# Kernel optimization log

Measured on AMD Instinct MI355X. Metric: run time of the kernel, lower is better.

## Reference

```python
import jax, jax.numpy as jnp
import numpy as np

NODES_PER_GRAPH = 1430  # hard-coded stride in the original forward
GENE0 = 1421            # first gene node index per graph
N_HEADS = 9


def gcn_conv(x, W, b, src, dst, n):
    """PyG-style GCNConv: D^-1/2 (A+I) D^-1/2 X W + b (self-loops added)."""
    h = x @ W  # [N, out]
    ones = jnp.ones(src.shape, jnp.float32)
    deg = jax.ops.segment_sum(ones, dst, num_segments=n) + 1.0  # +1 self-loop
    dinv = jax.lax.rsqrt(deg)
    norm = dinv[src] * dinv[dst]  # [E]
    agg = jax.ops.segment_sum(norm[:, None] * h[src], dst, num_segments=n)
    agg = agg + (dinv * dinv)[:, None] * h  # self-loop contribution
    return agg + b


def setup_inputs() -> dict:
    key = jax.random.key(0)
    ks = jax.random.split(key, 8)
    n_graphs = 512
    n = NODES_PER_GRAPH * n_graphs  # 732160 nodes
    e = n * 8                        # avg degree 8
    x = jax.random.normal(ks[0], (n, 1), jnp.float32)
    edge_index = jax.random.randint(ks[1], (2, e), 0, n, jnp.int32)
    y = jnp.zeros((n_graphs * N_HEADS,), jnp.int32)  # only y.size(0) is used
    W1 = jax.random.normal(ks[2], (1, 16), jnp.float32) * 0.5
    b1 = jnp.zeros((16,), jnp.float32)
    W2 = jax.random.normal(ks[3], (16, 16), jnp.float32) * 0.25
    b2 = jnp.zeros((16,), jnp.float32)
    fw1 = jax.random.normal(ks[4], (N_HEADS, 16, 8), jnp.float32) * 0.25
    fb1 = jnp.zeros((N_HEADS, 8), jnp.float32)
    fw2 = jax.random.normal(ks[5], (N_HEADS, 8, 1), jnp.float32) * 0.35
    fb2 = jnp.zeros((N_HEADS, 1), jnp.float32)
    return {"x": x, "edge_index": edge_index, "y": y, "W1": W1, "b1": b1,
            "W2": W2, "b2": b2, "fw1": fw1, "fb1": fb1, "fw2": fw2, "fb2": fb2}


def reference(x, edge_index, y, W1, b1, W2, b2, fw1, fb1, fw2, fb2):
    n = x.shape[0]
    src, dst = edge_index[0], edge_index[1]
    h = jax.nn.relu(gcn_conv(x, W1, b1, src, dst, n))
    # F.dropout(p=0.4) treated as identity (deterministic eval reference)
    h = jax.nn.relu(gcn_conv(h, W2, b2, src, dst, n))
    n_graphs = y.shape[0] // N_HEADS
    # fused version of the per-gene gather loop: idx[g, k] = 1421+g + k*1430
    idx = (GENE0 + jnp.arange(N_HEADS)[:, None]
           + jnp.arange(n_graphs)[None, :] * NODES_PER_GRAPH)  # [9, G]
    g = h[idx]  # [9, G, 16]
    z = jax.nn.relu(jnp.einsum('gnf,gfh->gnh', g, fw1) + fb1[:, None, :])
    pred = jnp.einsum('gnh,gho->gno', z, fw2) + fb2[:, None, :]  # [9, G, 1]
    return tuple(pred[i] for i in range(N_HEADS))
```

## Files before the change

### kernel.cpp

```cpp
#include <hip/hip_runtime.h>

#define NODES 1430
#define GENE0 1421
#define NHEADS 9
#define BHIST 1024
#define GMAX 64

__device__ __forceinline__ float frelu(float v) { return v > 0.f ? v : 0.f; }

__global__ __launch_bounds__(BHIST, 4)
void k_hist(const int* __restrict__ esrc, const int* __restrict__ edst,
            unsigned int* __restrict__ copies,
            int* __restrict__ gene_cnt, int* __restrict__ gene_src,
            unsigned int* __restrict__ flagw,
            int e, int K, int R, int n, int hbins, int hwords) {
    extern __shared__ unsigned int lds[];
    int id = blockIdx.x;
    int k, r;
    if ((K & 7) == 0) {
        int xcd = id & 7;
        int slot = id >> 3;
        int cin = slot / R;
        k = xcd * (K >> 3) + cin;
        r = slot - cin * R;
    } else {
        k = id / R;
        r = id - k * R;
    }
    const int tid = threadIdx.x;
    {
        uint4* l4 = (uint4*)lds;
        const int hw4 = hwords >> 2;
        for (int w = tid; w < hw4; w += BHIST) l4[w] = make_uint4(0, 0, 0, 0);
    }
    __syncthreads();

    const unsigned int lo = (unsigned int)r * (unsigned int)hbins;
    const unsigned int hb = (unsigned int)hbins;
    const int e4 = e >> 2;
    const int Q = (e4 + K - 1) / K;
    const int beg = k * Q;
    const int end = min(beg + Q, e4);
    const int4* ed4 = (const int4*)edst;
    const int len = (end > beg) ? (end - beg) : 0;
    const int eighth = len >> 3;

    auto proc = [&](int4 d4, int j4) {
#pragma unroll
        for (int c = 0; c < 4; c++) {
            unsigned int d = (unsigned int)((&d4.x)[c]);
            unsigned int rel = d - lo;
            if (rel < hb) {
                atomicAdd(&lds[rel >> 3], 1u << ((rel & 7u) * 4u));
                unsigned int graph = d / NODES;
                unsigned int pos = d - graph * NODES;
                if (pos >= GENE0) {
                    int s = esrc[4 * j4 + c];
                    atomicOr(&flagw[(unsigned)s >> 5], 1u << (s & 31));
                    int g = (int)(graph * NHEADS + (pos - GENE0));
                    int p = atomicAdd(gene_cnt + g, 1);
                    if (p < GMAX) gene_src[(g << 6) + p] = s;
                }
            }
        }
    };

    for (int i = tid; i < eighth; i += BHIST) {
        int j0 = beg + i;
        int4 v0 = ed4[j0];
        int4 v1 = ed4[j0 + eighth];
        int4 v2 = ed4[j0 + 2 * eighth];
        int4 v3 = ed4[j0 + 3 * eighth];
        int4 v4 = ed4[j0 + 4 * eighth];
        int4 v5 = ed4[j0 + 5 * eighth];
        int4 v6 = ed4[j0 + 6 * eighth];
        int4 v7 = ed4[j0 + 7 * eighth];
        proc(v0, j0);
        proc(v1, j0 + eighth);
        proc(v2, j0 + 2 * eighth);
        proc(v3, j0 + 3 * eighth);
        proc(v4, j0 + 4 * eighth);
        proc(v5, j0 + 5 * eighth);
        proc(v6, j0 + 6 * eighth);
        proc(v7, j0 + 7 * eighth);
    }
    for (int i = (eighth << 3) + tid; i < len; i += BHIST) {
        proc(ed4[beg + i], beg + i);
    }
    if (k == 0) {
        for (int j = (e4 << 2) + tid; j < e; j += BHIST) {
            unsigned int d = (unsigned int)edst[j];
            unsigned int rel = d - lo;
            if (rel < hb) {
                atomicAdd(&lds[rel >> 3], 1u << ((rel & 7u) * 4u));
                unsigned int graph = d / NODES;
                unsigned int pos = d - graph * NODES;
                if (pos >= GENE0) {
                    int s = esrc[j];
                    atomicOr(&flagw[(unsigned)s >> 5], 1u << (s & 31));
                    int g = (int)(graph * NHEADS + (pos - GENE0));
                    int p = atomicAdd(gene_cnt + g, 1);
                    if (p < GMAX) gene_src[(g << 6) + p] = s;
                }
            }
        }
    }
    __syncthreads();
    int wlimit = (n > (int)lo) ? ((n - (int)lo + 7) >> 3) : 0;
    if (wlimit > hwords) wlimit = hwords;
    int w4 = (wlimit + 3) >> 2;
    uint4* dst4 = (uint4*)(copies + ((size_t)k * R + r) * hwords);
    const uint4* l4 = (const uint4*)lds;
    for (int w = tid; w < w4; w += BHIST) dst4[w] = l4[w];
}

__global__ void k_reduce(const unsigned int* __restrict__ copies,
                         const float* __restrict__ x,
                         float2* __restrict__ dx, float* __restrict__ t,
                         int n, int K, int Wtot) {
    int w = blockIdx.x * blockDim.x + threadIdx.x;
    if (w >= Wtot) return;
    int i0 = w << 3;
    if (i0 >= n) return;
    const unsigned int M = 0x0F0F0F0Fu;
    unsigned int ev[8] = {0, 0, 0, 0, 0, 0, 0, 0};
    unsigned int od[8] = {0, 0, 0, 0, 0, 0, 0, 0};
    int k = 0;
    for (; k + 8 <= K; k += 8) {
#pragma unroll
        for (int s = 0; s < 8; s++) {
            unsigned int u = copies[(size_t)(k + s) * Wtot + w];
            ev[s] += u & M; od[s] += (u >> 4) & M;
        }
    }
    for (; k < K; k++) {
        unsigned int u = copies[(size_t)k * Wtot + w];
        ev[0] += u & M; od[0] += (u >> 4) & M;
    }
    unsigned int evn = ((ev[0] + ev[1]) + (ev[2] + ev[3])) + ((ev[4] + ev[5]) + (ev[6] + ev[7]));
    unsigned int odd = ((od[0] + od[1]) + (od[2] + od[3])) + ((od[4] + od[5]) + (od[6] + od[7]));
    float v[8];
#pragma unroll
    for (int b = 0; b < 4; b++) {
        v[2 * b]     = (float)((evn >> (8 * b)) & 0xFFu);
        v[2 * b + 1] = (float)((odd >> (8 * b)) & 0xFFu);
    }
#pragma unroll
    for (int b = 0; b < 8; b++) v[b] = rsqrtf(v[b] + 1.f);
    float4 z4 = {0.f, 0.f, 0.f, 0.f};
    if (i0 + 7 < n) {
        float4 xa = *(const float4*)(x + i0);
        float4 xb = *(const float4*)(x + i0 + 4);
        float4 p0 = {v[0], v[0] * xa.x, v[1], v[1] * xa.y};
        float4 p1 = {v[2], v[2] * xa.z, v[3], v[3] * xa.w};
        float4 p2 = {v[4], v[4] * xb.x, v[5], v[5] * xb.y};
        float4 p3 = {v[6], v[6] * xb.z, v[7], v[7] * xb.w};
        float4* dst = (float4*)(dx + i0);
        dst[0] = p0; dst[1] = p1; dst[2] = p2; dst[3] = p3;
        *(float4*)(t + i0) = z4;
        *(float4*)(t + i0 + 4) = z4;
    } else {
        for (int b = 0; b < 8; b++)
            if (i0 + b < n) {
                dx[i0 + b] = make_float2(v[b], v[b] * x[i0 + b]);
                t[i0 + b] = 0.f;
            }
    }
}

__global__ __launch_bounds__(256, 8)
void k_l1_scatter(const int* __restrict__ esrc, const int* __restrict__ edst,
                  const float2* __restrict__ dx,
                  const unsigned int* __restrict__ flagw,
                  float* __restrict__ t, int e) {
    const int4* ed4 = (const int4*)edst;
    const int e4 = e >> 2;
    const int tid = threadIdx.x;
    const int base = blockIdx.x * 2048 + tid;

    int4 dv[8];
#pragma unroll
    for (int k = 0; k < 8; k++) {
        int j = base + k * 256;
        dv[k] = (j < e4) ? ed4[j] : make_int4(-1, -1, -1, -1);
    }
    unsigned int hm[8];
#pragma unroll
    for (int k = 0; k < 8; k++) {
        unsigned int m = 0;
#pragma unroll
        for (int c = 0; c < 4; c++) {
            int d = (&dv[k].x)[c];
            unsigned int widx = (d >= 0) ? ((unsigned)d >> 5) : 0u;
            unsigned int fw = flagw[widx];
            if (d >= 0 && ((fw >> (d & 31)) & 1u)) m |= 1u << c;
        }
        hm[k] = m;
    }
#pragma unroll
    for (int k = 0; k < 8; k++) {
        if (hm[k]) {
            int j = base + k * 256;
#pragma unroll
            for (int c = 0; c < 4; c++) {
                if ((hm[k] >> c) & 1u) {
                    int s = esrc[4 * j + c];
                    atomicAdd(t + (&dv[k].x)[c], dx[s].y);
                }
            }
        }
    }
    if (blockIdx.x == 0) {
        for (int j = (e4 << 2) + tid; j < e; j += 256) {
            int d = edst[j];
            if ((flagw[(unsigned)d >> 5] >> (d & 31)) & 1u)
                atomicAdd(t + d, dx[esrc[j]].y);
        }
    }
}

__global__ void k_gene_final(const int* __restrict__ gene_cnt, const int* __restrict__ gene_src,
                             const float* __restrict__ t, const float2* __restrict__ dx,
                             const float* __restrict__ W1, const float* __restrict__ b1,
                             const float* __restrict__ W2, const float* __restrict__ b2,
                             const float* __restrict__ fw1, const float* __restrict__ fb1,
                             const float* __restrict__ fw2, const float* __restrict__ fb2,
                             float* __restrict__ out, int NG, int G) {
    int wid = (blockIdx.x * blockDim.x + threadIdx.x) >> 6;
    int lane = threadIdx.x & 63;
    if (wid >= NG) return;
    int g = wid;
    int graph = g / NHEADS;
    int head = g - graph * NHEADS;
    int node = graph * NODES + GENE0 + head;
    const int c = lane & 15;
    const int slot = lane >> 4;
    int cnt = min(gene_cnt[g], GMAX);

    float w1r[16], b1r[16], w2c[16];
#pragma unroll
    for (int kk = 0; kk < 16; kk++) {
        w1r[kk] = W1[kk];
        b1r[kk] = b1[kk];
        w2c[kk] = W2[kk * 16 + c];
    }
    float2 dn2 = dx[node];

    float acc = 0.f, tsum = 0.f;
    const int base = g << 6;
    for (int i = slot; i < cnt; i += 8) {
        int s0 = gene_src[base + i];
        int i1 = i + 4;
        int s1 = (i1 < cnt) ? gene_src[base + i1] : -1;
        float2 a2 = dx[s0];
        float ta = t[s0];
        float2 b2v = (s1 >= 0) ? dx[s1] : make_float2(0.f, 0.f);
        float tb = (s1 >= 0) ? t[s1] : 0.f;
        tsum += a2.y + b2v.y;
        {
            float us = a2.x * ta + a2.x * a2.y;
            float m = 0.f;
#pragma unroll
            for (int kk = 0; kk < 16; kk++)
                m += frelu(us * w1r[kk] + b1r[kk]) * w2c[kk];
            acc += a2.x * m;
        }
        if (s1 >= 0) {
            float us = b2v.x * tb + b2v.x * b2v.y;
            float m = 0.f;
#pragma unroll
            for (int kk = 0; kk < 16; kk++)
                m += frelu(us * w1r[kk] + b1r[kk]) * w2c[kk];
            acc += b2v.x * m;
        }
    }
    acc += __shfl_xor(acc, 16, 64);
    acc += __shfl_xor(acc, 32, 64);
    tsum += __shfl_xor(tsum, 16, 64);
    tsum += __shfl_xor(tsum, 32, 64);

    float dn = dn2.x;
    float un = dn * tsum + dn * dn2.y;
    float h2 = 0.f;
#pragma unroll
    for (int kk = 0; kk < 16; kk++)
        h2 += frelu(un * w1r[kk] + b1r[kk]) * w2c[kk];
    float h = frelu(dn * acc + dn * dn * h2 + b2[c]);

    float hv[16];
#pragma unroll
    for (int c2 = 0; c2 < 16; c2++) hv[c2] = __shfl(h, c2, 64);

    int kk = lane & 7;
    float z = fb1[head * 8 + kk];
#pragma unroll
    for (int c2 = 0; c2 < 16; c2++) z += hv[c2] * fw1[head * 128 + c2 * 8 + kk];
    float term = frelu(z) * fw2[head * 8 + kk];
    term += __shfl_xor(term, 1, 64);
    term += __shfl_xor(term, 2, 64);
    term += __shfl_xor(term, 4, 64);
    if (lane == 0) out[head * G + graph] = fb2[head] + term;
}

extern "C" void kernel_launch(void* const* d_in, const int* in_sizes, int n_in,
                              void* d_out, int out_size, void* d_ws, size_t ws_size,
                              hipStream_t stream) {
    const float* x   = (const float*)d_in[0];
    const int*   ei  = (const int*)d_in[1];
    const float* W1  = (const float*)d_in[3];
    const float* b1  = (const float*)d_in[4];
    const float* W2  = (const float*)d_in[5];
    const float* b2  = (const float*)d_in[6];
    const float* fw1 = (const float*)d_in[7];
    const float* fb1 = (const float*)d_in[8];
    const float* fw2 = (const float*)d_in[9];
    const float* fb2 = (const float*)d_in[10];

    int n = in_sizes[0];
    int e = in_sizes[1] / 2;
    int G = in_sizes[2] / NHEADS;
    int NG = G * NHEADS;
    const int* esrc = ei;
    const int* edst = ei + e;
    int nw = (n + 31) / 32;

    static int HB_RT = 0;
    if (HB_RT == 0) {
        hipError_t st = hipFuncSetAttribute(
            reinterpret_cast<const void*>(k_hist),
            hipFuncAttributeMaxDynamicSharedMemorySize, 131072);
        HB_RT = (st == hipSuccess) ? 262144 : 131072;
    }
    const int HB = HB_RT;
    const int HW = HB >> 3;

    char* ws = (char*)d_ws;
    size_t off = 0;
    auto alloc = [&](size_t bytes) {
        char* p = ws + off;
        off += (bytes + 255) & ~(size_t)255;
        return p;
    };
    int*   gene_cnt      = (int*)alloc((size_t)NG * 4);
    unsigned int* flagw  = (unsigned int*)alloc((size_t)nw * 4);
    size_t zero_bytes    = off;
    int*    gene_src     = (int*)alloc((size_t)NG * GMAX * 4);
    float*  t            = (float*)alloc((size_t)n * 4);
    float2* dx           = (float2*)alloc((size_t)n * 8);
    size_t fixed         = off;

    int R = (n + HB - 1) / HB;
    size_t per_copy = (size_t)R * HW * 4;
    int K = 80;
    if (fixed + (size_t)K * per_copy > ws_size) {
        size_t avail = (ws_size > fixed) ? (ws_size - fixed) : 0;
        int kfit = (int)(avail / per_copy);
        if (kfit >= 8) kfit &= ~7;
        K = kfit < 1 ? 1 : (kfit < K ? kfit : K);
    }
    unsigned int* copies = (unsigned int*)alloc((size_t)K * per_copy);
    (void)n_in; (void)out_size;

    hipMemsetAsync(d_ws, 0, zero_bytes, stream);

    const int B = 256;
    size_t shmem = (size_t)HW * 4;
    k_hist<<<K * R, BHIST, shmem, stream>>>(esrc, edst, copies, gene_cnt, gene_src,
                                            flagw, e, K, R, n, HB, HW);
    int Wtot = R * HW;
    k_reduce<<<(Wtot + B - 1) / B, B, 0, stream>>>(copies, x, dx, t, n, K, Wtot);
    int e4 = e >> 2;
    int nblk = (e4 + 2047) / 2048;
    k_l1_scatter<<<nblk, 256, 0, stream>>>(esrc, edst, dx, flagw, t, e);
    int waves_blocks = (NG * 64 + B - 1) / B;
    k_gene_final<<<waves_blocks, B, 0, stream>>>(gene_cnt, gene_src, t, dx,
                                                 W1, b1, W2, b2,
                                                 fw1, fb1, fw2, fb2,
                                                 (float*)d_out, NG, G);
}
```

Baseline: 191.0 us.

## Precompute gene-neighbor flags and compact flagged edges during histogram pass

```diff
diff --git a/kernel.cpp b/kernel.cpp
--- a/kernel.cpp
+++ b/kernel.cpp
@@ -5,16 +5,88 @@
 #define NHEADS 9
 #define BHIST 1024
 #define GMAX 64
+#define BCAP 8192
 
 __device__ __forceinline__ float frelu(float v) { return v > 0.f ? v : 0.f; }
+
+__global__ __launch_bounds__(256, 8)
+void k_pre(const int* __restrict__ esrc, const int* __restrict__ edst,
+           int* __restrict__ gene_cnt, int* __restrict__ gene_src,
+           unsigned int* __restrict__ flagw, int e) {
+    const int tid = threadIdx.x;
+    const int e4 = e >> 2;
+    const int nb = gridDim.x;
+    const int Q = (e4 + nb - 1) / nb;
+    const int beg = blockIdx.x * Q;
+    const int end = min(beg + Q, e4);
+    const int len = (end > beg) ? (end - beg) : 0;
+    const int4* ed4 = (const int4*)edst;
+    const int eighth = len >> 3;
+
+    auto proc = [&](int4 d4, int j4) {
+#pragma unroll
+        for (int c = 0; c < 4; c++) {
+            unsigned int d = (unsigned int)((&d4.x)[c]);
+            unsigned int graph = d / NODES;
+            unsigned int pos = d - graph * NODES;
+            if (pos >= GENE0) {
+                int s = esrc[4 * j4 + c];
+                atomicOr(&flagw[(unsigned)s >> 5], 1u << (s & 31));
+                int g = (int)(graph * NHEADS + (pos - GENE0));
+                int p = atomicAdd(gene_cnt + g, 1);
+                if (p < GMAX) gene_src[(g << 6) + p] = s;
+            }
+        }
+    };
+
+    for (int i = tid; i < eighth; i += 256) {
+        int j0 = beg + i;
+        int4 v0 = ed4[j0];
+        int4 v1 = ed4[j0 + eighth];
+        int4 v2 = ed4[j0 + 2 * eighth];
+        int4 v3 = ed4[j0 + 3 * eighth];
+        int4 v4 = ed4[j0 + 4 * eighth];
+        int4 v5 = ed4[j0 + 5 * eighth];
+        int4 v6 = ed4[j0 + 6 * eighth];
+        int4 v7 = ed4[j0 + 7 * eighth];
+        proc(v0, j0);
+        proc(v1, j0 + eighth);
+        proc(v2, j0 + 2 * eighth);
+        proc(v3, j0 + 3 * eighth);
+        proc(v4, j0 + 4 * eighth);
+        proc(v5, j0 + 5 * eighth);
+        proc(v6, j0 + 6 * eighth);
+        proc(v7, j0 + 7 * eighth);
+    }
+    for (int i = (eighth << 3) + tid; i < len; i += 256) {
+        proc(ed4[beg + i], beg + i);
+    }
+    if (blockIdx.x == 0) {
+        for (int j = (e4 << 2) + tid; j < e; j += 256) {
+            unsigned int d = (unsigned int)edst[j];
+            unsigned int graph = d / NODES;
+            unsigned int pos = d - graph * NODES;
+            if (pos >= GENE0) {
+                int s = esrc[j];
+                atomicOr(&flagw[(unsigned)s >> 5], 1u << (s & 31));
+                int g = (int)(graph * NHEADS + (pos - GENE0));
+                int p = atomicAdd(gene_cnt + g, 1);
+                if (p < GMAX) gene_src[(g << 6) + p] = s;
+            }
+        }
+    }
+}
 
 __global__ __launch_bounds__(BHIST, 4)
 void k_hist(const int* __restrict__ esrc, const int* __restrict__ edst,
             unsigned int* __restrict__ copies,
-            int* __restrict__ gene_cnt, int* __restrict__ gene_src,
-            unsigned int* __restrict__ flagw,
+            const unsigned int* __restrict__ flagw,
+            int2* __restrict__ hits,
+            int* __restrict__ bcnt,
+            unsigned int* __restrict__ ocnt, int2* __restrict__ ohits,
             int e, int K, int R, int n, int hbins, int hwords) {
     extern __shared__ unsigned int lds[];
+    __shared__ int bqn;
     int id = blockIdx.x;
     int k, r;
     if ((K & 7) == 0) {
@@ -33,8 +105,10 @@
         const int hw4 = hwords >> 2;
         for (int w = tid; w < hw4; w += BHIST) l4[w] = make_uint4(0, 0, 0, 0);
     }
+    if (tid == 0) bqn = 0;
     __syncthreads();
 
+    int2* blkq = hits + (size_t)id * BCAP;
     const unsigned int lo = (unsigned int)r * (unsigned int)hbins;
     const unsigned int hb = (unsigned int)hbins;
     const int e4 = e >> 2;
@@ -52,14 +126,12 @@
             unsigned int rel = d - lo;
             if (rel < hb) {
                 atomicAdd(&lds[rel >> 3], 1u << ((rel & 7u) * 4u));
-                unsigned int graph = d / NODES;
-                unsigned int pos = d - graph * NODES;
-                if (pos >= GENE0) {
+                if ((flagw[d >> 5] >> (d & 31)) & 1u) {
                     int s = esrc[4 * j4 + c];
-                    atomicOr(&flagw[(unsigned)s >> 5], 1u << (s & 31));
-                    int g = (int)(graph * NHEADS + (pos - GENE0));
-                    int p = atomicAdd(gene_cnt + g, 1);
-                    if (p < GMAX) gene_src[(g << 6) + p] = s;
+                    int2 v = make_int2(s, (int)d);
+                    int idx = atomicAdd(&bqn, 1);
+                    if (idx < BCAP) blkq[idx] = v;
+                    else { unsigned op = atomicAdd(ocnt, 1u); ohits[op] = v; }
                 }
             }
         }
@@ -93,19 +165,18 @@
             unsigned int rel = d - lo;
             if (rel < hb) {
                 atomicAdd(&lds[rel >> 3], 1u << ((rel & 7u) * 4u));
-                unsigned int graph = d / NODES;
-                unsigned int pos = d - graph * NODES;
-                if (pos >= GENE0) {
+                if ((flagw[d >> 5] >> (d & 31)) & 1u) {
                     int s = esrc[j];
-                    atomicOr(&flagw[(unsigned)s >> 5], 1u << (s & 31));
-                    int g = (int)(graph * NHEADS + (pos - GENE0));
-                    int p = atomicAdd(gene_cnt + g, 1);
-                    if (p < GMAX) gene_src[(g << 6) + p] = s;
+                    int2 v = make_int2(s, (int)d);
+                    int idx = atomicAdd(&bqn, 1);
+                    if (idx < BCAP) blkq[idx] = v;
+                    else { unsigned op = atomicAdd(ocnt, 1u); ohits[op] = v; }
                 }
             }
         }
     }
     __syncthreads();
+    if (tid == 0) bcnt[id] = min(bqn, BCAP);
     int wlimit = (n > (int)lo) ? ((n - (int)lo + 7) >> 3) : 0;
     if (wlimit > hwords) wlimit = hwords;
     int w4 = (wlimit + 3) >> 2;
@@ -169,52 +240,23 @@
 }
 
 __global__ __launch_bounds__(256, 8)
-void k_l1_scatter(const int* __restrict__ esrc, const int* __restrict__ edst,
-                  const float2* __restrict__ dx,
-                  const unsigned int* __restrict__ flagw,
-                  float* __restrict__ t, int e) {
-    const int4* ed4 = (const int4*)edst;
-    const int e4 = e >> 2;
-    const int tid = threadIdx.x;
-    const int base = blockIdx.x * 2048 + tid;
-
-    int4 dv[8];
-#pragma unroll
-    for (int k = 0; k < 8; k++) {
-        int j = base + k * 256;
-        dv[k] = (j < e4) ? ed4[j] : make_int4(-1, -1, -1, -1);
-    }
-    unsigned int hm[8];
-#pragma unroll
-    for (int k = 0; k < 8; k++) {
-        unsigned int m = 0;
-#pragma unroll
-        for (int c = 0; c < 4; c++) {
-            int d = (&dv[k].x)[c];
-            unsigned int widx = (d >= 0) ? ((unsigned)d >> 5) : 0u;
-            unsigned int fw = flagw[widx];
-            if (d >= 0 && ((fw >> (d & 31)) & 1u)) m |= 1u << c;
-        }
-        hm[k] = m;
-    }
-#pragma unroll
-    for (int k = 0; k < 8; k++) {
-        if (hm[k]) {
-            int j = base + k * 256;
-#pragma unroll
-            for (int c = 0; c < 4; c++) {
-                if ((hm[k] >> c) & 1u) {
-                    int s = esrc[4 * j + c];
-                    atomicAdd(t + (&dv[k].x)[c], dx[s].y);
-                }
-            }
-        }
-    }
-    if (blockIdx.x == 0) {
-        for (int j = (e4 << 2) + tid; j < e; j += 256) {
-            int d = edst[j];
-            if ((flagw[(unsigned)d >> 5] >> (d & 31)) & 1u)
-                atomicAdd(t + d, dx[esrc[j]].y);
+void k_drain(const int2* __restrict__ hits, const int* __restrict__ bcnt,
+             const int2* __restrict__ ohits, const unsigned int* __restrict__ ocnt,
+             const float2* __restrict__ dx, float* __restrict__ t, int nbh) {
+    int b = blockIdx.x;
+    if (b < nbh) {
+        int m = bcnt[b];
+        const int2* rg = hits + (size_t)b * BCAP;
+        for (int i = threadIdx.x; i < m; i += 256) {
+            int2 sd = rg[i];
+            atomicAdd(t + sd.y, dx[sd.x].y);
+        }
+    } else {
+        int m = (int)*ocnt;
+        int stride = (gridDim.x - nbh) * 256;
+        for (int i = (b - nbh) * 256 + threadIdx.x; i < m; i += stride) {
+            int2 sd = ohits[i];
+            atomicAdd(t + sd.y, dx[sd.x].y);
         }
     }
 }
@@ -343,6 +385,7 @@
     };
     int*   gene_cnt      = (int*)alloc((size_t)NG * 4);
     unsigned int* flagw  = (unsigned int*)alloc((size_t)nw * 4);
+    unsigned int* ocnt   = (unsigned int*)alloc(4);
     size_t zero_bytes    = off;
     int*    gene_src     = (int*)alloc((size_t)NG * GMAX * 4);
     float*  t            = (float*)alloc((size_t)n * 4);
@@ -352,26 +395,31 @@
     int R = (n + HB - 1) / HB;
     size_t per_copy = (size_t)R * HW * 4;
     int K = 80;
-    if (fixed + (size_t)K * per_copy > ws_size) {
-        size_t avail = (ws_size > fixed) ? (ws_size - fixed) : 0;
+    size_t extra = (size_t)K * R * BCAP * 8 + (size_t)K * R * 4 + (size_t)e * 8 + 1024;
+    if (fixed + (size_t)K * per_copy + extra > ws_size) {
+        size_t avail = (ws_size > fixed + extra) ? (ws_size - fixed - extra) : 0;
         int kfit = (int)(avail / per_copy);
         if (kfit >= 8) kfit &= ~7;
         K = kfit < 1 ? 1 : (kfit < K ? kfit : K);
     }
+    int NBH = K * R;
     unsigned int* copies = (unsigned int*)alloc((size_t)K * per_copy);
+    int2* hits           = (int2*)alloc((size_t)NBH * BCAP * 8);
+    int*  bcnt           = (int*)alloc((size_t)NBH * 4);
+    int2* ohits          = (int2*)alloc((size_t)e * 8);
     (void)n_in; (void)out_size;
 
     hipMemsetAsync(d_ws, 0, zero_bytes, stream);
 
     const int B = 256;
+    k_pre<<<512, 256, 0, stream>>>(esrc, edst, gene_cnt, gene_src, flagw, e);
     size_t shmem = (size_t)HW * 4;
-    k_hist<<<K * R, BHIST, shmem, stream>>>(esrc, edst, copies, gene_cnt, gene_src,
-                                            flagw, e, K, R, n, HB, HW);
+    k_hist<<<NBH, BHIST, shmem, stream>>>(esrc, edst, copies, flagw,
+                                          hits, bcnt, ocnt, ohits,
+                                          e, K, R, n, HB, HW);
     int Wtot = R * HW;
     k_reduce<<<(Wtot + B - 1) / B, B, 0, stream>>>(copies, x, dx, t, n, K, Wtot);
-    int e4 = e >> 2;
-    int nblk = (e4 + 2047) / 2048;
-    k_l1_scatter<<<nblk, 256, 0, stream>>>(esrc, edst, dx, flagw, t, e);
+    k_drain<<<NBH + 8, 256, 0, stream>>>(hits, bcnt, ohits, ocnt, dx, t, NBH);
     int waves_blocks = (NG * 64 + B - 1) / B;
     k_gene_final<<<waves_blocks, B, 0, stream>>>(gene_cnt, gene_src, t, dx,
                                                  W1, b1, W2, b2,
```

Result: slower. 238.6 us (+24.9%).
